# Performance work log

Hardware: AMD Instinct MI355X
Metric: run time of the kernel (lower is better)

Reference implementation:

```python
import jax, jax.numpy as jnp
import numpy as np

B, S, D, H, DH = 4, 2048, 512, 16, 32  # d_model=512, head_num=16, d_head=32


def setup_inputs() -> dict:
    key = jax.random.key(0)
    ks = jax.random.split(key, 9)
    scale = 0.02
    return {
        "x": jax.random.normal(ks[0], (B, S, D), dtype=jnp.float32),
        "Wq": jax.random.normal(ks[1], (H, D, DH), dtype=jnp.float32) * scale,
        "bq": jax.random.normal(ks[2], (H, DH), dtype=jnp.float32) * scale,
        "Wk": jax.random.normal(ks[3], (H, D, DH), dtype=jnp.float32) * scale,
        "bk": jax.random.normal(ks[4], (H, DH), dtype=jnp.float32) * scale,
        "Wv": jax.random.normal(ks[5], (H, D, DH), dtype=jnp.float32) * scale,
        "bv": jax.random.normal(ks[6], (H, DH), dtype=jnp.float32) * scale,
        "Wo": jax.random.normal(ks[7], (D, D), dtype=jnp.float32) * scale,
        "bo": jax.random.normal(ks[8], (D,), dtype=jnp.float32) * scale,
    }


def reference(x, Wq, bq, Wk, bk, Wv, bv, Wo, bo):
    # Batched per-head projections (equivalent to the 3*H separate Linears).
    q = jnp.einsum('bsd,hdk->bhsk', x, Wq) + bq[:, None, :]  # [B,H,S,DH]
    k = jnp.einsum('bsd,hdk->bhsk', x, Wk) + bk[:, None, :]
    v = jnp.einsum('bsd,hdk->bhsk', x, Wv) + bv[:, None, :]
    # Scaled dot-product attention per head (no mask: original forward never
    # forwards its mask argument into calculate_Score).
    scores = jnp.einsum('bhsk,bhtk->bhst', q, k) / jnp.sqrt(jnp.float32(DH))
    attn = jax.nn.softmax(scores, axis=-1)
    z = jnp.einsum('bhst,bhtk->bhsk', attn, v)  # [B,H,S,DH]
    # Concatenate heads: cat([z_0..z_{H-1}], dim=-1) == transpose+reshape.
    multihead = jnp.transpose(z, (0, 2, 1, 3)).reshape(B, S, D)
    # Output projection (torch Linear: y = x @ W.T + b).
    return multihead @ Wo.T + bo
```

## Files before the change

kernel.cpp:

```cpp
#include <hip/hip_runtime.h>
#include <hip/hip_bf16.h>
#include <math.h>

#define BB 4
#define SS 2048
#define DD 512
#define HH 16
#define DHH 32
#define SCL_Q 0.25505402528478404f

typedef __bf16 bf16x8  __attribute__((ext_vector_type(8)));
typedef __bf16 bf16x4v __attribute__((ext_vector_type(4)));
typedef float  f32x2   __attribute__((ext_vector_type(2)));
typedef float  f32x4   __attribute__((ext_vector_type(4)));
typedef float  f32x16  __attribute__((ext_vector_type(16)));
typedef unsigned int u32;

#if __has_builtin(__builtin_amdgcn_exp2f)
#define EXP2F __builtin_amdgcn_exp2f
#else
#define EXP2F exp2f
#endif

static __device__ __forceinline__ f32x4 mfma16(bf16x8 a, bf16x8 b, f32x4 c) {
    return __builtin_amdgcn_mfma_f32_16x16x32_bf16(a, b, c, 0, 0, 0);
}
static __device__ __forceinline__ f32x16 mfma32(bf16x8 a, bf16x8 b, f32x16 c) {
    return __builtin_amdgcn_mfma_f32_32x32x16_bf16(a, b, c, 0, 0, 0);
}
static __device__ __forceinline__ f32x16 zero16() {
    f32x16 z;
    #pragma unroll
    for (int i = 0; i < 16; ++i) z[i] = 0.f;
    return z;
}

static __device__ __forceinline__ void half_swap(u32 &a, u32 &b) {
#if __has_builtin(__builtin_amdgcn_permlane32_swap)
    auto r = __builtin_amdgcn_permlane32_swap(a, b, false, false);
    a = (u32)r[0]; b = (u32)r[1];
#else
    const int hi_ = (threadIdx.x & 32) != 0;
    const u32 sa = (u32)__shfl_xor((int)a, 32);
    const u32 sb = (u32)__shfl_xor((int)b, 32);
    const u32 na = hi_ ? sb : a;
    const u32 nb = hi_ ? b : sa;
    a = na; b = nb;
#endif
}
static __device__ __forceinline__ float xor32_add(float x) {
    u32 a = __float_as_uint(x), b = a;
    half_swap(a, b);
    return __uint_as_float(a) + __uint_as_float(b);
}
static __device__ __forceinline__ u32 pack_bf16(float lo_, float hi_) {
    union { __bf16 h[2]; u32 u; } p;
    p.h[0] = (__bf16)lo_;
    p.h[1] = (__bf16)hi_;
    return p.u;
}

union V16 { f32x16 v; f32x2 h[8]; float f[16]; };

__global__ __launch_bounds__(256) void convert_k(
    const float* __restrict__ x,
    const float* __restrict__ Wq, const float* __restrict__ Wk, const float* __restrict__ Wv,
    const float* __restrict__ Wo,
    __bf16* __restrict__ xbf, __bf16* __restrict__ wt, __bf16* __restrict__ wob)
{
    const int bid = blockIdx.x;
    const int t = threadIdx.x;
    if (bid < 1024) {
        for (int i = bid * 256 + t; i < 1048576; i += 1024 * 256) {
            float4 v = ((const float4*)x)[i];
            bf16x4v pk;
            pk[0] = (__bf16)v.x; pk[1] = (__bf16)v.y; pk[2] = (__bf16)v.z; pk[3] = (__bf16)v.w;
            ((bf16x4v*)xbf)[i] = pk;
        }
    } else if (bid < 1216) {
        const int id = bid - 1024;
        const int mat = id / 64, rem = id % 64;
        const int h = rem >> 2, dseg = rem & 3;
        const float* W = (mat == 0) ? Wq : (mat == 1) ? Wk : Wv;
        const float sc = (mat == 0) ? SCL_Q : 1.0f;
        const int dloc = t & 127, half = t >> 7;
        const int d = dseg * 128 + dloc;
        const float* src = W + ((size_t)h * DD + d) * DHH + half * 16;
        __bf16* dst = wt + (size_t)(mat * HH + h) * DHH * DD + (size_t)half * 16 * DD + d;
        float vals[16];
        #pragma unroll
        for (int q = 0; q < 4; ++q) {
            float4 v4 = *(const float4*)(src + q * 4);
            vals[q*4+0] = v4.x; vals[q*4+1] = v4.y; vals[q*4+2] = v4.z; vals[q*4+3] = v4.w;
        }
        #pragma unroll
        for (int j = 0; j < 16; ++j)
            dst[(size_t)j * DD] = (__bf16)(vals[j] * sc);
    } else {
        const int id = bid - 1216;
        for (int i = id * 256 + t; i < 65536; i += 64 * 256) {
            float4 v = ((const float4*)Wo)[i];
            bf16x4v pk;
            pk[0] = (__bf16)v.x; pk[1] = (__bf16)v.y; pk[2] = (__bf16)v.z; pk[3] = (__bf16)v.w;
            ((bf16x4v*)wob)[i] = pk;
        }
    }
}

__global__ __launch_bounds__(256) void qkv_mfma_k(
    const __bf16* __restrict__ xbf, const __bf16* __restrict__ wt,
    const float* __restrict__ bq, const float* __restrict__ bk, const float* __restrict__ bv,
    __bf16* __restrict__ qb, __bf16* __restrict__ kb, __bf16* __restrict__ vtb)
{
    const int t = threadIdx.x;
    const int w = t >> 6, L = t & 63;
    const int wm = w & 1, wn = w >> 1;
    const int m_base = blockIdx.y * 128 + wm * 64;
    const int n_base = blockIdx.x * 128 + wn * 64;
    const int mat = n_base >> 9;

    if (mat == 2) {
        const int lo = L & 31, hi2 = L >> 5;
        const int hb = (blockIdx.x & 3) * 4 + (wn << 1);
        f32x16 accv[2][2];
        #pragma unroll
        for (int tm = 0; tm < 2; ++tm)
            #pragma unroll
            for (int nt = 0; nt < 2; ++nt) accv[tm][nt] = zero16();

        const __bf16* ap0 = xbf + (size_t)(m_base + lo) * DD + hi2 * 8;
        const __bf16* ap1 = ap0 + (size_t)32 * DD;
        const __bf16* bp0 = wt + ((size_t)(2 * HH + hb) * DHH + lo) * DD + hi2 * 8;
        const __bf16* bp1 = bp0 + (size_t)DHH * DD;

        for (int k0 = 0; k0 < DD; k0 += 16) {
            bf16x8 x0 = *(const bf16x8*)(ap0 + k0);
            bf16x8 x1 = *(const bf16x8*)(ap1 + k0);
            bf16x8 w0 = *(const bf16x8*)(bp0 + k0);
            bf16x8 w1 = *(const bf16x8*)(bp1 + k0);
            accv[0][0] = mfma32(w0, x0, accv[0][0]);
            accv[0][1] = mfma32(w1, x0, accv[0][1]);
            accv[1][0] = mfma32(w0, x1, accv[1][0]);
            accv[1][1] = mfma32(w1, x1, accv[1][1]);
        }

        #pragma unroll
        for (int tm = 0; tm < 2; ++tm) {
            const int m0t = m_base + tm * 32;
            const int b = m0t >> 11, ss = m0t & (SS - 1);
            #pragma unroll
            for (int nt = 0; nt < 2; ++nt) {
                const int head = hb + nt;
                #pragma unroll
                for (int r = 0; r < 16; ++r) {
                    const int d = (r & 3) + 8 * (r >> 2) + 4 * hi2;
                    const float bias = bv[head * DHH + d];
                    vtb[((size_t)(b * HH + head) * DHH + d) * SS + ss + lo] =
                        (__bf16)(accv[tm][nt][r] + bias);
                }
            }
        }
        return;
    }

    const int lo = L & 15, g = L >> 4;
    const __bf16* aptr[4];
    const __bf16* bptr[4];
    int headA[4], dhbA[4];
    #pragma unroll
    for (int fi = 0; fi < 4; ++fi)
        aptr[fi] = xbf + (size_t)(m_base + fi * 16 + lo) * DD + g * 8;
    #pragma unroll
    for (int fj = 0; fj < 4; ++fj) {
        const int nl = (n_base + fj * 16) & 511;
        headA[fj] = nl >> 5;
        dhbA[fj] = nl & 31;
        bptr[fj] = wt + ((size_t)(mat * HH + headA[fj]) * DHH + dhbA[fj] + lo) * DD + g * 8;
    }

    f32x4 acc[4][4];
    #pragma unroll
    for (int fi = 0; fi < 4; ++fi)
        #pragma unroll
        for (int fj = 0; fj < 4; ++fj)
            acc[fi][fj] = f32x4{0.f, 0.f, 0.f, 0.f};

    for (int k0 = 0; k0 < DD; k0 += 32) {
        bf16x8 a[4], bfr[4];
        #pragma unroll
        for (int fi = 0; fi < 4; ++fi) a[fi] = *(const bf16x8*)(aptr[fi] + k0);
        #pragma unroll
        for (int fj = 0; fj < 4; ++fj) bfr[fj] = *(const bf16x8*)(bptr[fj] + k0);
        #pragma unroll
        for (int fi = 0; fi < 4; ++fi)
            #pragma unroll
            for (int fj = 0; fj < 4; ++fj)
                acc[fi][fj] = mfma16(bfr[fj], a[fi], acc[fi][fj]);
    }

    const float* bias_p = (mat == 0) ? bq : bk;
    __bf16* outqk = (mat == 0) ? qb : kb;
    #pragma unroll
    for (int fj = 0; fj < 4; ++fj) {
        const int head = headA[fj];
        const int dh0 = dhbA[fj] + g * 4;
        float4 b4 = *(const float4*)(bias_p + head * DHH + dh0);
        if (mat == 0) { b4.x *= SCL_Q; b4.y *= SCL_Q; b4.z *= SCL_Q; b4.w *= SCL_Q; }
        #pragma unroll
        for (int fi = 0; fi < 4; ++fi) {
            const int m = m_base + fi * 16 + lo;
            const int b = m >> 11, ss = m & (SS - 1);
            bf16x4v pk;
            pk[0] = (__bf16)(acc[fi][fj][0] + b4.x);
            pk[1] = (__bf16)(acc[fi][fj][1] + b4.y);
            pk[2] = (__bf16)(acc[fi][fj][2] + b4.z);
            pk[3] = (__bf16)(acc[fi][fj][3] + b4.w);
            *(bf16x4v*)(outqk + ((size_t)(b * HH + head) * SS + ss) * DHH + dh0) = pk;
        }
    }
}

__global__ __launch_bounds__(64, 2) void attn_k(
    const __bf16* __restrict__ qb, const __bf16* __restrict__ kb,
    const __bf16* __restrict__ vtb, __bf16* __restrict__ mh)
{
    const int L = threadIdx.x & 63;
    const int lo = L & 31, hi = L >> 5;
    const int wg = blockIdx.x;
    const int xcd = wg & 7, rr = wg >> 3;
    const int qp = rr & 31;
    const int bh = xcd + ((rr >> 5) << 3);
    const int b = bh >> 4, h = bh & 15;

    const size_t qkbase = (size_t)bh * SS * DHH;
    const int Rb1 = qp * 32;
    const int Rb2 = Rb1 + 1024;

    bf16x8 qf1[2], qf2[2];
    #pragma unroll
    for (int ds = 0; ds < 2; ++ds) {
        qf1[ds] = *(const bf16x8*)(qb + qkbase + (size_t)(Rb1 + lo) * DHH + ds * 16 + hi * 8);
        qf2[ds] = *(const bf16x8*)(qb + qkbase + (size_t)(Rb2 + lo) * DHH + ds * 16 + hi * 8);
    }

    V16 o1, o2;
    o1.v = zero16();
    o2.v = zero16();
    float l1 = 0.f, l2 = 0.f;

    const __bf16* kbp = kb + qkbase;
    const __bf16* vbp = vtb + (size_t)bh * DHH * SS + (size_t)lo * SS;

    bf16x8 kA[4], kB[4];
    {
        const __bf16* kr0 = kbp + (size_t)lo * DHH;
        const __bf16* kr1 = kr0 + 32 * DHH;
        kA[0] = *(const bf16x8*)(kr0 + hi * 8);
        kA[1] = *(const bf16x8*)(kr0 + 16 + hi * 8);
        kA[2] = *(const bf16x8*)(kr1 + hi * 8);
        kA[3] = *(const bf16x8*)(kr1 + 16 + hi * 8);
    }

    auto qset = [&](bf16x8 (&kc)[4], bf16x8 (&qf)[2], bf16x8 (&vf)[2][2],
                    V16 &o, float &l_run) {
        __builtin_amdgcn_s_setprio(1);
        V16 S0, S1;
        S0.v = mfma32(kc[0], qf[0], zero16());
        S0.v = mfma32(kc[1], qf[1], S0.v);
        S1.v = mfma32(kc[2], qf[0], zero16());
        S1.v = mfma32(kc[3], qf[1], S1.v);
        __builtin_amdgcn_s_setprio(0);

        #pragma unroll
        for (int j = 0; j < 16; ++j) S0.f[j] = EXP2F(S0.f[j]);
        #pragma unroll
        for (int j = 0; j < 16; ++j) S1.f[j] = EXP2F(S1.f[j]);

        f32x2 u[8];
        #pragma unroll
        for (int i = 0; i < 8; ++i) u[i] = S0.h[i] + S1.h[i];
        #pragma unroll
        for (int d = 4; d > 0; d >>= 1)
            #pragma unroll
            for (int i = 0; i < d; ++i) u[i] += u[i + d];
        l_run += xor32_add(u[0][0] + u[0][1]);

        #pragma unroll
        for (int kg = 0; kg < 2; ++kg) {
            u32 c[4][2];
            #pragma unroll
            for (int n = 0; n < 4; ++n)
                #pragma unroll
                for (int m = 0; m < 2; ++m) {
                    const int ip = 2 * n + m;
                    c[n][m] = (kg == 0) ? pack_bf16(S0.h[ip][0], S0.h[ip][1])
                                        : pack_bf16(S1.h[ip][0], S1.h[ip][1]);
                }
            __builtin_amdgcn_s_setprio(1);
            #pragma unroll
            for (int ks = 0; ks < 2; ++ks) {
                u32 a0 = c[2 * ks][0], b0 = c[2 * ks + 1][0];
                u32 a1 = c[2 * ks][1], b1 = c[2 * ks + 1][1];
                half_swap(a0, b0);
                half_swap(a1, b1);
                union { u32 u[4]; bf16x8 v; } pu;
                pu.u[0] = a0; pu.u[1] = a1; pu.u[2] = b0; pu.u[3] = b1;
                o.v = mfma32(vf[kg][ks], pu.v, o.v);
            }
            __builtin_amdgcn_s_setprio(0);
        }
    };

    auto body = [&](int kt, bf16x8 (&kc)[4], bf16x8 (&kn)[4]) {
        const int k0 = kt * 64;
        {
            const int ktn = (kt < 31) ? kt + 1 : 31;
            const __bf16* nr0 = kbp + (size_t)(ktn * 64 + lo) * DHH;
            const __bf16* nr1 = nr0 + 32 * DHH;
            kn[0] = *(const bf16x8*)(nr0 + hi * 8);
            kn[1] = *(const bf16x8*)(nr0 + 16 + hi * 8);
            kn[2] = *(const bf16x8*)(nr1 + hi * 8);
            kn[3] = *(const bf16x8*)(nr1 + 16 + hi * 8);
        }
        bf16x8 vf[2][2];
        #pragma unroll
        for (int kg = 0; kg < 2; ++kg)
            #pragma unroll
            for (int ks = 0; ks < 2; ++ks)
                vf[kg][ks] = *(const bf16x8*)(vbp + k0 + kg * 32 + ks * 16 + hi * 8);

        qset(kc, qf1, vf, o1, l1);
        qset(kc, qf2, vf, o2, l2);
    };

    for (int kt2 = 0; kt2 < 32; kt2 += 2) {
        body(kt2,     kA, kB);
        body(kt2 + 1, kB, kA);
    }

    {
        const float inv = 1.0f / l1;
        __bf16* op = mh + ((size_t)b * SS + Rb1 + lo) * DD + h * DHH + 4 * hi;
        #pragma unroll
        for (int n = 0; n < 4; ++n) {
            bf16x4v pk;
            #pragma unroll
            for (int j = 0; j < 4; ++j) pk[j] = (__bf16)(o1.f[4 * n + j] * inv);
            *(bf16x4v*)(op + 8 * n) = pk;
        }
    }
    {
        const float inv = 1.0f / l2;
        __bf16* op = mh + ((size_t)b * SS + Rb2 + lo) * DD + h * DHH + 4 * hi;
        #pragma unroll
        for (int n = 0; n < 4; ++n) {
            bf16x4v pk;
            #pragma unroll
            for (int j = 0; j < 4; ++j) pk[j] = (__bf16)(o2.f[4 * n + j] * inv);
            *(bf16x4v*)(op + 8 * n) = pk;
        }
    }
}

__global__ __launch_bounds__(64, 4) void oproj_k(
    const __bf16* __restrict__ mh, const __bf16* __restrict__ wob,
    const float* __restrict__ bo, float* __restrict__ y)
{
    const int L = threadIdx.x & 63;
    const int lo = L & 31, hi = L >> 5;
    const int n0 = blockIdx.x * 32;
    const int m0 = blockIdx.y * 32;

    const __bf16* ap = mh  + (size_t)(m0 + lo) * DD + hi * 8;
    const __bf16* bp = wob + (size_t)(n0 + lo) * DD + hi * 8;

    f32x16 acc = zero16();
    #pragma unroll 4
    for (int ks = 0; ks < 32; ++ks) {
        bf16x8 a = *(const bf16x8*)(ap + ks * 16);
        bf16x8 b = *(const bf16x8*)(bp + ks * 16);
        acc = mfma32(b, a, acc);
    }

    const int m = m0 + lo;
    #pragma unroll
    for (int g2 = 0; g2 < 4; ++g2) {
        const int n = n0 + 8 * g2 + 4 * hi;
        const float4 b4 = *(const float4*)(bo + n);
        float4 ov;
        ov.x = acc[4 * g2 + 0] + b4.x;
        ov.y = acc[4 * g2 + 1] + b4.y;
        ov.z = acc[4 * g2 + 2] + b4.z;
        ov.w = acc[4 * g2 + 3] + b4.w;
        *(float4*)(y + (size_t)m * DD + n) = ov;
    }
}

extern "C" void kernel_launch(void* const* d_in, const int* in_sizes, int n_in,
                              void* d_out, int out_size, void* d_ws, size_t ws_size,
                              hipStream_t stream) {
    const float* x  = (const float*)d_in[0];
    const float* Wq = (const float*)d_in[1];
    const float* bq = (const float*)d_in[2];
    const float* Wk = (const float*)d_in[3];
    const float* bk = (const float*)d_in[4];
    const float* Wv = (const float*)d_in[5];
    const float* bv = (const float*)d_in[6];
    const float* Wo = (const float*)d_in[7];
    const float* bo = (const float*)d_in[8];
    float* y = (float*)d_out;

    char* wsb = (char*)d_ws;
    __bf16* xbf  = (__bf16*)(wsb);
    __bf16* qbuf = (__bf16*)(wsb +  8388608);
    __bf16* kbuf = (__bf16*)(wsb + 16777216);
    __bf16* vtb  = (__bf16*)(wsb + 25165824);
    __bf16* mhb  = (__bf16*)(wsb + 33554432);
    __bf16* wt   = (__bf16*)(wsb + 41943040);
    __bf16* wob  = (__bf16*)(wsb + 43515904);

    convert_k <<<1280, 256, 0, stream>>>(x, Wq, Wk, Wv, Wo, xbf, wt, wob);
    qkv_mfma_k<<<dim3(12, 64), 256, 0, stream>>>(xbf, wt, bq, bk, bv, qbuf, kbuf, vtb);
    attn_k    <<<dim3(2048),    64, 0, stream>>>(qbuf, kbuf, vtb, mhb);
    oproj_k   <<<dim3(16, 256), 64, 0, stream>>>(mhb, wob, bo, y);
}
```

Before: 173.6 us.

## Process four query sets per attention wave and add MFMA priority hints

The attention kernel now gives each wave four 32-row query blocks instead of two. Each loaded K/V tile is reused across more queries, and the grid halves to 1024 single-wave blocks with launch bounds relaxed to allow more registers. The QKV and output-projection GEMM loops wrap their MFMAs in s_setprio, and oproj splits its accumulator in two to break the MFMA dependency chain. The cost is higher register pressure and fewer waves, which may reduce occupancy and latency hiding in attention.

After: 160.7 us. 7.4% less time.

```diff
diff --git a/kernel.cpp b/kernel.cpp
--- a/kernel.cpp
+++ b/kernel.cpp
@@ -138,10 +138,12 @@
             bf16x8 x1 = *(const bf16x8*)(ap1 + k0);
             bf16x8 w0 = *(const bf16x8*)(bp0 + k0);
             bf16x8 w1 = *(const bf16x8*)(bp1 + k0);
+            __builtin_amdgcn_s_setprio(1);
             accv[0][0] = mfma32(w0, x0, accv[0][0]);
             accv[0][1] = mfma32(w1, x0, accv[0][1]);
             accv[1][0] = mfma32(w0, x1, accv[1][0]);
             accv[1][1] = mfma32(w1, x1, accv[1][1]);
+            __builtin_amdgcn_s_setprio(0);
         }
 
         #pragma unroll
@@ -191,11 +193,13 @@
         for (int fi = 0; fi < 4; ++fi) a[fi] = *(const bf16x8*)(aptr[fi] + k0);
         #pragma unroll
         for (int fj = 0; fj < 4; ++fj) bfr[fj] = *(const bf16x8*)(bptr[fj] + k0);
+        __builtin_amdgcn_s_setprio(1);
         #pragma unroll
         for (int fi = 0; fi < 4; ++fi)
             #pragma unroll
             for (int fj = 0; fj < 4; ++fj)
                 acc[fi][fj] = mfma16(bfr[fj], a[fi], acc[fi][fj]);
+        __builtin_amdgcn_s_setprio(0);
     }
 
     const float* bias_p = (mat == 0) ? bq : bk;
@@ -220,7 +224,7 @@
     }
 }
 
-__global__ __launch_bounds__(64, 2) void attn_k(
+__global__ __launch_bounds__(64, 1) void attn_k(
     const __bf16* __restrict__ qb, const __bf16* __restrict__ kb,
     const __bf16* __restrict__ vtb, __bf16* __restrict__ mh)
 {
@@ -228,25 +232,25 @@
     const int lo = L & 31, hi = L >> 5;
     const int wg = blockIdx.x;
     const int xcd = wg & 7, rr = wg >> 3;
-    const int qp = rr & 31;
-    const int bh = xcd + ((rr >> 5) << 3);
+    const int qp = rr & 15;
+    const int bh = xcd + ((rr >> 4) << 3);
     const int b = bh >> 4, h = bh & 15;
 
     const size_t qkbase = (size_t)bh * SS * DHH;
-    const int Rb1 = qp * 32;
-    const int Rb2 = Rb1 + 1024;
-
-    bf16x8 qf1[2], qf2[2];
-    #pragma unroll
-    for (int ds = 0; ds < 2; ++ds) {
-        qf1[ds] = *(const bf16x8*)(qb + qkbase + (size_t)(Rb1 + lo) * DHH + ds * 16 + hi * 8);
-        qf2[ds] = *(const bf16x8*)(qb + qkbase + (size_t)(Rb2 + lo) * DHH + ds * 16 + hi * 8);
-    }
-
-    V16 o1, o2;
-    o1.v = zero16();
-    o2.v = zero16();
-    float l1 = 0.f, l2 = 0.f;
+
+    bf16x8 qf[4][2];
+    #pragma unroll
+    for (int qs = 0; qs < 4; ++qs) {
+        const int Rb = qp * 32 + qs * 512;
+        #pragma unroll
+        for (int ds = 0; ds < 2; ++ds)
+            qf[qs][ds] = *(const bf16x8*)(qb + qkbase + (size_t)(Rb + lo) * DHH + ds * 16 + hi * 8);
+    }
+
+    V16 o[4];
+    float lr[4];
+    #pragma unroll
+    for (int qs = 0; qs < 4; ++qs) { o[qs].v = zero16(); lr[qs] = 0.f; }
 
     const __bf16* kbp = kb + qkbase;
     const __bf16* vbp = vtb + (size_t)bh * DHH * SS + (size_t)lo * SS;
@@ -261,14 +265,14 @@
         kA[3] = *(const bf16x8*)(kr1 + 16 + hi * 8);
     }
 
-    auto qset = [&](bf16x8 (&kc)[4], bf16x8 (&qf)[2], bf16x8 (&vf)[2][2],
-                    V16 &o, float &l_run) {
+    auto qset = [&](bf16x8 (&kc)[4], bf16x8 (&qfr)[2], bf16x8 (&vf)[2][2],
+                    V16 &oo, float &l_run) {
         __builtin_amdgcn_s_setprio(1);
         V16 S0, S1;
-        S0.v = mfma32(kc[0], qf[0], zero16());
-        S0.v = mfma32(kc[1], qf[1], S0.v);
-        S1.v = mfma32(kc[2], qf[0], zero16());
-        S1.v = mfma32(kc[3], qf[1], S1.v);
+        S0.v = mfma32(kc[0], qfr[0], zero16());
+        S0.v = mfma32(kc[1], qfr[1], S0.v);
+        S1.v = mfma32(kc[2], qfr[0], zero16());
+        S1.v = mfma32(kc[3], qfr[1], S1.v);
         __builtin_amdgcn_s_setprio(0);
 
         #pragma unroll
@@ -305,7 +309,7 @@
                 half_swap(a1, b1);
                 union { u32 u[4]; bf16x8 v; } pu;
                 pu.u[0] = a0; pu.u[1] = a1; pu.u[2] = b0; pu.u[3] = b1;
-                o.v = mfma32(vf[kg][ks], pu.v, o.v);
+                oo.v = mfma32(vf[kg][ks], pu.v, oo.v);
             }
             __builtin_amdgcn_s_setprio(0);
         }
@@ -329,8 +333,9 @@
             for (int ks = 0; ks < 2; ++ks)
                 vf[kg][ks] = *(const bf16x8*)(vbp + k0 + kg * 32 + ks * 16 + hi * 8);
 
-        qset(kc, qf1, vf, o1, l1);
-        qset(kc, qf2, vf, o2, l2);
+        #pragma unroll
+        for (int qs = 0; qs < 4; ++qs)
+            qset(kc, qf[qs], vf, o[qs], lr[qs]);
     };
 
     for (int kt2 = 0; kt2 < 32; kt2 += 2) {
@@ -338,25 +343,16 @@
         body(kt2 + 1, kB, kA);
     }
 
-    {
-        const float inv = 1.0f / l1;
-        __bf16* op = mh + ((size_t)b * SS + Rb1 + lo) * DD + h * DHH + 4 * hi;
+    #pragma unroll
+    for (int qs = 0; qs < 4; ++qs) {
+        const int Rb = qp * 32 + qs * 512;
+        const float inv = 1.0f / lr[qs];
+        __bf16* op = mh + ((size_t)b * SS + Rb + lo) * DD + h * DHH + 4 * hi;
         #pragma unroll
         for (int n = 0; n < 4; ++n) {
             bf16x4v pk;
             #pragma unroll
-            for (int j = 0; j < 4; ++j) pk[j] = (__bf16)(o1.f[4 * n + j] * inv);
-            *(bf16x4v*)(op + 8 * n) = pk;
-        }
-    }
-    {
-        const float inv = 1.0f / l2;
-        __bf16* op = mh + ((size_t)b * SS + Rb2 + lo) * DD + h * DHH + 4 * hi;
-        #pragma unroll
-        for (int n = 0; n < 4; ++n) {
-            bf16x4v pk;
-            #pragma unroll
-            for (int j = 0; j < 4; ++j) pk[j] = (__bf16)(o2.f[4 * n + j] * inv);
+            for (int j = 0; j < 4; ++j) pk[j] = (__bf16)(o[qs].f[4 * n + j] * inv);
             *(bf16x4v*)(op + 8 * n) = pk;
         }
     }
@@ -374,12 +370,22 @@
     const __bf16* ap = mh  + (size_t)(m0 + lo) * DD + hi * 8;
     const __bf16* bp = wob + (size_t)(n0 + lo) * DD + hi * 8;
 
-    f32x16 acc = zero16();
-    #pragma unroll 4
-    for (int ks = 0; ks < 32; ++ks) {
-        bf16x8 a = *(const bf16x8*)(ap + ks * 16);
-        bf16x8 b = *(const bf16x8*)(bp + ks * 16);
-        acc = mfma32(b, a, acc);
+    f32x16 acc0 = zero16(), acc1 = zero16();
+    for (int ks = 0; ks < 32; ks += 4) {
+        bf16x8 a0 = *(const bf16x8*)(ap + (ks + 0) * 16);
+        bf16x8 b0 = *(const bf16x8*)(bp + (ks + 0) * 16);
+        bf16x8 a1 = *(const bf16x8*)(ap + (ks + 1) * 16);
+        bf16x8 b1 = *(const bf16x8*)(bp + (ks + 1) * 16);
+        bf16x8 a2 = *(const bf16x8*)(ap + (ks + 2) * 16);
+        bf16x8 b2 = *(const bf16x8*)(bp + (ks + 2) * 16);
+        bf16x8 a3 = *(const bf16x8*)(ap + (ks + 3) * 16);
+        bf16x8 b3 = *(const bf16x8*)(bp + (ks + 3) * 16);
+        __builtin_amdgcn_s_setprio(1);
+        acc0 = mfma32(b0, a0, acc0);
+        acc1 = mfma32(b1, a1, acc1);
+        acc0 = mfma32(b2, a2, acc0);
+        acc1 = mfma32(b3, a3, acc1);
+        __builtin_amdgcn_s_setprio(0);
     }
 
     const int m = m0 + lo;
@@ -388,10 +394,10 @@
         const int n = n0 + 8 * g2 + 4 * hi;
         const float4 b4 = *(const float4*)(bo + n);
         float4 ov;
-        ov.x = acc[4 * g2 + 0] + b4.x;
-        ov.y = acc[4 * g2 + 1] + b4.y;
-        ov.z = acc[4 * g2 + 2] + b4.z;
-        ov.w = acc[4 * g2 + 3] + b4.w;
+        ov.x = acc0[4 * g2 + 0] + acc1[4 * g2 + 0] + b4.x;
+        ov.y = acc0[4 * g2 + 1] + acc1[4 * g2 + 1] + b4.y;
+        ov.z = acc0[4 * g2 + 2] + acc1[4 * g2 + 2] + b4.z;
+        ov.w = acc0[4 * g2 + 3] + acc1[4 * g2 + 3] + b4.w;
         *(float4*)(y + (size_t)m * DD + n) = ov;
     }
 }
@@ -421,6 +427,6 @@
 
     convert_k <<<1280, 256, 0, stream>>>(x, Wq, Wk, Wv, Wo, xbf, wt, wob);
     qkv_mfma_k<<<dim3(12, 64), 256, 0, stream>>>(xbf, wt, bq, bk, bv, qbuf, kbuf, vtb);
-    attn_k    <<<dim3(2048),    64, 0, stream>>>(qbuf, kbuf, vtb, mhb);
+    attn_k    <<<dim3(1024),    64, 0, stream>>>(qbuf, kbuf, vtb, mhb);
     oproj_k   <<<dim3(16, 256), 64, 0, stream>>>(mhb, wob, bo, y);
 }
```
